# Optimization experiments

Measured on AMD Instinct MI355X. Metric: run time of the kernel, lower is better.

The kernel has to match this reference:

```python
import jax, jax.numpy as jnp
import numpy as np

N, E = 100000, 1600000          # nodes, edges
H, DH = 8, 256                  # heads, dim_hidden
D = DH // H                     # dim per head
NEG_SLOPE = 0.2                 # GAT leaky_relu slope
BETA = 0.5


def setup_inputs() -> dict:
    key = jax.random.key(0)
    ks = jax.random.split(key, 10)
    s = 1.0 / np.sqrt(DH)
    return {
        "x": jax.random.normal(ks[0], (N, DH), jnp.float32),
        "edge_index": jax.random.randint(ks[1], (2, E), 0, N, jnp.int32),
        "edge_attr": jax.random.uniform(ks[2], (E,), jnp.float32),
        # GAT params (no bias, add_self_loops=False)
        "Wg": jax.random.normal(ks[3], (DH, DH), jnp.float32) * s,
        "att_src": jax.random.normal(ks[4], (H, D), jnp.float32) * s,
        "att_dst": jax.random.normal(ks[5], (H, D), jnp.float32) * s,
        # h_lin
        "Wh": jax.random.normal(ks[6], (DH, DH), jnp.float32) * s,
        "bh": jnp.zeros((DH,), jnp.float32),
        # lin
        "Wl": jax.random.normal(ks[7], (DH, DH), jnp.float32) * s,
        "bl": jnp.zeros((DH,), jnp.float32),
        # LayerNorm
        "ln_g": jnp.ones((DH,), jnp.float32),
        "ln_b": jnp.zeros((DH,), jnp.float32),
        # beta gate (beta>=0 -> constant vector)
        "b_param": jnp.full((DH,), BETA, jnp.float32),
    }


def _layer_norm(v, g, b, eps=1e-5):
    mu = jnp.mean(v, axis=-1, keepdims=True)
    var = jnp.var(v, axis=-1, keepdims=True)
    return (v - mu) * jax.lax.rsqrt(var + eps) * g + b


def _weighted_gat(x, edge_index, edge_attr, Wg, att_src, att_dst):
    # GATConv with per-edge weights folded into the softmax numerator.
    xs = (x @ Wg).reshape(N, H, D)                       # [N,H,D]
    a_src = jnp.einsum("nhd,hd->nh", xs, att_src)        # [N,H]
    a_dst = jnp.einsum("nhd,hd->nh", xs, att_dst)
    src, dst = edge_index[0], edge_index[1]
    e = jax.nn.leaky_relu(a_src[src] + a_dst[dst], NEG_SLOPE)   # [E,H]
    m = jax.ops.segment_max(e, dst, num_segments=N)             # [N,H]
    m = jnp.where(jnp.isfinite(m), m, 0.0)                      # isolated nodes
    p = jnp.exp(e - m[dst]) * edge_attr[:, None]                # weighted exp
    denom = jax.ops.segment_sum(p, dst, num_segments=N)         # [N,H]
    alpha = p / (denom[dst] + 1e-16)                            # [E,H]
    msg = alpha[:, :, None] * xs[src]                           # [E,H,D]
    out = jax.ops.segment_sum(msg, dst, num_segments=N)         # [N,H,D]
    return out.reshape(N, DH)


def reference(x, edge_index, edge_attr, Wg, att_src, att_dst, Wh, bh, Wl, bl, ln_g, ln_b, b_param):
    x_in = x
    h = jax.nn.relu(x @ Wh + bh)
    xg = _weighted_gat(x, edge_index, edge_attr, Wg, att_src, att_dst) + (x @ Wl + bl)
    xg = jax.nn.relu(xg)                                  # dropout p=0 (eval)
    beta = b_param[None, :]
    out = (1.0 - beta) * _layer_norm(h * xg, ln_g, ln_b) + beta * xg
    return out + x_in                                     # residual=True
```

## Files before the change

### kernel.cpp

```cpp
#include <hip/hip_runtime.h>

typedef __attribute__((ext_vector_type(4))) float f32x4;
typedef __attribute__((ext_vector_type(8))) __bf16 bf16x8;

__device__ __forceinline__ unsigned short f2bf(float f) {
    return __builtin_bit_cast(unsigned short, (__bf16)f);
}
__device__ __forceinline__ float bf2f(unsigned short u) {
    return __builtin_bit_cast(float, (unsigned)u << 16);
}

__device__ __forceinline__ void gload16(const void* g, void* l) {
    __builtin_amdgcn_global_load_lds(
        (const __attribute__((address_space(1))) void*)g,
        (__attribute__((address_space(3))) void*)l, 16, 0, 0);
}

__global__ __launch_bounds__(256) void k_prep(
    const float* __restrict__ x, unsigned short* __restrict__ xb, long total, long totalPad,
    const float* __restrict__ Wg, const float* __restrict__ Wh, const float* __restrict__ Wl,
    unsigned short* __restrict__ wt,
    const int* __restrict__ dst, int E, int* __restrict__ deg,
    int nCvt, int nHist) {
    const int b = blockIdx.x;
    const int tid = threadIdx.x;
    if (b < nCvt) {
        long i = ((long)b * 256 + tid) * 4;
        if (i >= totalPad) return;
        if (i < total) {
            float4 v = *(const float4*)(x + i);
            ushort4 u;
            u.x = f2bf(v.x); u.y = f2bf(v.y); u.z = f2bf(v.z); u.w = f2bf(v.w);
            *(ushort4*)(xb + i) = u;
        } else {
            ushort4 u = {0, 0, 0, 0};
            *(ushort4*)(xb + i) = u;
        }
    } else if (b < nCvt + 768) {
        int t = (b - nCvt) * 256 + tid;
        int nn = t >> 8, k = t & 255;
        const float* W = (nn < 256) ? Wg : (nn < 512) ? Wh : Wl;
        wt[t] = f2bf(W[k * 256 + (nn & 255)]);
    } else {
        int bb = b - nCvt - 768;
        for (int e = bb * 256 + tid; e < E; e += nHist * 256)
            atomicAdd(&deg[dst[e]], 1);
    }
}

__global__ __launch_bounds__(256) void k_gemm(
    const unsigned short* __restrict__ A,
    const unsigned short* __restrict__ BT,
    unsigned short* __restrict__ xs, unsigned short* __restrict__ hb,
    unsigned short* __restrict__ xlb,
    const float* __restrict__ bh, const float* __restrict__ bl, int M, int nwg) {
    __shared__ unsigned short Al[128 * 32];
    __shared__ unsigned short Bl[128 * 32];
    const int bid = blockIdx.x;
    const int xcd = bid & 7, idx = bid >> 3;
    const int q = nwg >> 3, r = nwg & 7;
    const int wg = (xcd < r ? xcd * (q + 1) : r * (q + 1) + (xcd - r) * q) + idx;
    const int tm = wg / 6, tn = wg % 6;

    const int tid = threadIdx.x;
    const int lane = tid & 63;
    const int wave = tid >> 6;
    const int wm = (wave >> 1) * 64, wn = (wave & 1) * 64;

    f32x4 acc[4][4] = {};

    const int r0 = tid >> 2;
    const int ce = (tid & 3) * 8;
    const unsigned short* Ag = A + (size_t)tm * 128 * 256 + (size_t)r0 * 256 + ce;
    const unsigned short* Bg = BT + (size_t)tn * 128 * 256 + (size_t)r0 * 256 + ce;

    const int fr = lane & 15;
    const int ko = (lane >> 4) * 8;

    for (int ks = 0; ks < 8; ++ks) {
        const int k0 = ks * 32;
#pragma unroll
        for (int s = 0; s < 2; ++s) {
            gload16(Ag + (size_t)s * 64 * 256 + k0, (char*)Al + s * 4096 + wave * 1024);
            gload16(Bg + (size_t)s * 64 * 256 + k0, (char*)Bl + s * 4096 + wave * 1024);
        }
        __syncthreads();
        bf16x8 af[4], bfr[4];
#pragma unroll
        for (int i = 0; i < 4; ++i) {
            af[i]  = *(const bf16x8*)&Al[(wm + i * 16 + fr) * 32 + ko];
            bfr[i] = *(const bf16x8*)&Bl[(wn + i * 16 + fr) * 32 + ko];
        }
#pragma unroll
        for (int i = 0; i < 4; ++i)
#pragma unroll
            for (int j = 0; j < 4; ++j)
                acc[i][j] = __builtin_amdgcn_mfma_f32_16x16x32_bf16(af[i], bfr[j], acc[i][j], 0, 0, 0);
        __syncthreads();
    }

    const int colbase = tn * 128 + wn;
    const int rbase = tm * 128 + wm + (lane >> 4) * 4;
#pragma unroll
    for (int i = 0; i < 4; ++i) {
#pragma unroll
        for (int j = 0; j < 4; ++j) {
            const int cg = colbase + j * 16 + (lane & 15);
#pragma unroll
            for (int q2 = 0; q2 < 4; ++q2) {
                const int rg = rbase + i * 16 + q2;
                if (rg < M) {
                    float v = acc[i][j][q2];
                    if (cg < 256) {
                        xs[(size_t)rg * 256 + cg] = f2bf(v);
                    } else if (cg < 512) {
                        float t = v + bh[cg - 256];
                        hb[(size_t)rg * 256 + (cg - 256)] = f2bf(t > 0.f ? t : 0.f);
                    } else {
                        xlb[(size_t)rg * 256 + (cg - 512)] = f2bf(v + bl[cg - 512]);
                    }
                }
            }
        }
    }
}

__global__ __launch_bounds__(256) void k_attn(const unsigned short* __restrict__ xs,
                                              const float* __restrict__ att_src,
                                              const float* __restrict__ att_dst,
                                              float* __restrict__ a_src,
                                              float* __restrict__ a_dst, int N) {
    int t = blockIdx.x * 256 + threadIdx.x;
    int n = t >> 3, hh = t & 7;
    if (n >= N) return;
    const ushort4* xp = (const ushort4*)(xs + (size_t)n * 256 + hh * 32);
    const float4* sp = (const float4*)(att_src + hh * 32);
    const float4* dp = (const float4*)(att_dst + hh * 32);
    float sa = 0.f, sd = 0.f;
#pragma unroll
    for (int q = 0; q < 8; ++q) {
        ushort4 u = xp[q];
        float4 s = sp[q], d = dp[q];
        float v0 = bf2f(u.x), v1 = bf2f(u.y), v2 = bf2f(u.z), v3 = bf2f(u.w);
        sa += v0 * s.x + v1 * s.y + v2 * s.z + v3 * s.w;
        sd += v0 * d.x + v1 * d.y + v2 * d.z + v3 * d.w;
    }
    a_src[t] = sa;
    a_dst[t] = sd;
}

__global__ __launch_bounds__(256) void k_scan1(const int* __restrict__ deg, int* __restrict__ offs,
                                               int* __restrict__ bsum, int Npad) {
    __shared__ int s[256];
    int t = threadIdx.x;
    int i = blockIdx.x * 256 + t;
    int v = (i < Npad) ? deg[i] : 0;
    s[t] = v;
    __syncthreads();
#pragma unroll
    for (int off = 1; off < 256; off <<= 1) {
        int x = (t >= off) ? s[t - off] : 0;
        __syncthreads();
        s[t] += x;
        __syncthreads();
    }
    offs[i] = s[t] - v;
    if (t == 255) bsum[blockIdx.x] = s[255];
}

__global__ __launch_bounds__(512) void k_scan2(int* __restrict__ bsum, int nb) {
    __shared__ int s[512];
    int t = threadIdx.x;
    int v = (t < nb) ? bsum[t] : 0;
    s[t] = v;
    __syncthreads();
#pragma unroll
    for (int off = 1; off < 512; off <<= 1) {
        int x = (t >= off) ? s[t - off] : 0;
        __syncthreads();
        s[t] += x;
        __syncthreads();
    }
    if (t < nb) bsum[t] = s[t] - v;
}

__global__ __launch_bounds__(256) void k_scan3(int* __restrict__ offs, const int* __restrict__ bsum,
                                               int* __restrict__ cursor) {
    int i = blockIdx.x * 256 + threadIdx.x;
    int o = offs[i] + bsum[blockIdx.x];
    offs[i] = o;
    cursor[i] = o;
}

__global__ void k_edge(const int* __restrict__ ei, const float* __restrict__ ea, int E,
                       const float* __restrict__ a_src, const float* __restrict__ a_dst,
                       int* __restrict__ cursor, int* __restrict__ srcArr,
                       unsigned short* __restrict__ pvArr) {
    for (int e = blockIdx.x * blockDim.x + threadIdx.x; e < E; e += gridDim.x * blockDim.x) {
        const int s = ei[e];
        const int d = ei[(size_t)E + e];
        const float w = ea[e];
        const int pos = atomicAdd(&cursor[d], 1);
        const float4* As = (const float4*)(a_src + (size_t)s * 8);
        const float4* Ad = (const float4*)(a_dst + (size_t)d * 8);
        float4 s0 = As[0], s1 = As[1], d0 = Ad[0], d1 = Ad[1];
        float a[8] = {s0.x + d0.x, s0.y + d0.y, s0.z + d0.z, s0.w + d0.w,
                      s1.x + d1.x, s1.y + d1.y, s1.z + d1.z, s1.w + d1.w};
        unsigned pk[4];
#pragma unroll
        for (int h = 0; h < 4; ++h) {
            float lo = a[2 * h], hi = a[2 * h + 1];
            lo = (lo > 0.f) ? lo : 0.2f * lo;
            hi = (hi > 0.f) ? hi : 0.2f * hi;
            unsigned short plo = f2bf(__expf(lo) * w);
            unsigned short phi = f2bf(__expf(hi) * w);
            pk[h] = (unsigned)plo | ((unsigned)phi << 16);
        }
        srcArr[pos] = s;
        uint4 v = {pk[0], pk[1], pk[2], pk[3]};
        *(uint4*)(pvArr + (size_t)pos * 8) = v;
    }
}

__global__ __launch_bounds__(256) void k_agg(
    const int* __restrict__ offs, const int* __restrict__ deg,
    const int* __restrict__ srcArr, const unsigned short* __restrict__ pvArr,
    const unsigned short* __restrict__ xs, const unsigned short* __restrict__ hb,
    const unsigned short* __restrict__ xlb,
    const float* __restrict__ x, const float* __restrict__ ln_g, const float* __restrict__ ln_b,
    const float* __restrict__ beta, float* __restrict__ out, int N) {
    const int wave = threadIdx.x >> 6, lane = threadIdx.x & 63;
    const int n = blockIdx.x * 4 + wave;
    if (n >= N) return;
    const int start = __builtin_amdgcn_readfirstlane(offs[n]);
    const int dcount = __builtin_amdgcn_readfirstlane(deg[n]);
    const int head = lane >> 3;

    f32x4 acc = {0.f, 0.f, 0.f, 0.f};
    float dsum = 0.f;

    const int* sp = srcArr + start;
    const unsigned short* pp = pvArr + (size_t)start * 8 + head;
    const char* xsb = (const char*)xs;
    const unsigned rowoff = (unsigned)lane * 8;

    for (int e0 = 0; e0 < dcount; e0 += 8) {
        const int cnt = dcount - e0;
        int srcs[8];
        float pvv[8];
        ushort4 rows[8];
#pragma unroll
        for (int e = 0; e < 8; ++e)
            if (e < cnt) srcs[e] = sp[e0 + e];
#pragma unroll
        for (int e = 0; e < 8; ++e)
            if (e < cnt) {
                pvv[e] = bf2f(pp[(size_t)(e0 + e) * 8]);
                rows[e] = *(const ushort4*)(xsb + (size_t)(unsigned)srcs[e] * 512 + rowoff);
            }
#pragma unroll
        for (int e = 0; e < 8; ++e)
            if (e < cnt) {
                const float p = pvv[e];
                dsum += p;
                acc[0] += p * bf2f(rows[e].x);
                acc[1] += p * bf2f(rows[e].y);
                acc[2] += p * bf2f(rows[e].z);
                acc[3] += p * bf2f(rows[e].w);
            }
    }
    const float inv = 1.f / (dsum + 1e-16f);

    const size_t base = (size_t)n * 256 + lane * 4;
    ushort4 xlu = *(const ushort4*)(xlb + base);
    ushort4 hu = *(const ushort4*)(hb + base);
    f32x4 xg, t4;
    float s1 = 0.f, s2 = 0.f;
    const float xl0[4] = {bf2f(xlu.x), bf2f(xlu.y), bf2f(xlu.z), bf2f(xlu.w)};
    const float hv0[4] = {bf2f(hu.x), bf2f(hu.y), bf2f(hu.z), bf2f(hu.w)};
#pragma unroll
    for (int q = 0; q < 4; ++q) {
        float gg = acc[q] * inv + xl0[q];
        gg = gg > 0.f ? gg : 0.f;
        xg[q] = gg;
        float t = hv0[q] * gg;
        t4[q] = t;
        s1 += t;
        s2 += t * t;
    }
#pragma unroll
    for (int off = 32; off; off >>= 1) {
        s1 += __shfl_xor(s1, off);
        s2 += __shfl_xor(s2, off);
    }
    const float mu = s1 * (1.f / 256.f);
    const float var = s2 * (1.f / 256.f) - mu * mu;
    const float rs = rsqrtf(var + 1e-5f);

    f32x4 g4 = *(const f32x4*)(ln_g + lane * 4);
    f32x4 b4 = *(const f32x4*)(ln_b + lane * 4);
    f32x4 be = *(const f32x4*)(beta + lane * 4);
    f32x4 xin = *(const f32x4*)(x + base);
    f32x4 o;
#pragma unroll
    for (int q = 0; q < 4; ++q) {
        float ln = (t4[q] - mu) * rs * g4[q] + b4[q];
        o[q] = (1.f - be[q]) * ln + be[q] * xg[q] + xin[q];
    }
    *(f32x4*)(out + base) = o;
}

extern "C" void kernel_launch(void* const* d_in, const int* in_sizes, int n_in,
                              void* d_out, int out_size, void* d_ws, size_t ws_size,
                              hipStream_t stream) {
    const float* x = (const float*)d_in[0];
    const int* ei = (const int*)d_in[1];
    const float* ea = (const float*)d_in[2];
    const float* Wg = (const float*)d_in[3];
    const float* att_src = (const float*)d_in[4];
    const float* att_dst = (const float*)d_in[5];
    const float* Wh = (const float*)d_in[6];
    const float* bh = (const float*)d_in[7];
    const float* Wl = (const float*)d_in[8];
    const float* bl = (const float*)d_in[9];
    const float* ln_g = (const float*)d_in[10];
    const float* ln_b = (const float*)d_in[11];
    const float* beta = (const float*)d_in[12];
    float* out = (float*)d_out;

    const int DH = 256;
    const int N = in_sizes[0] / DH;
    const int E = in_sizes[2];
    const int Mpad = ((N + 127) / 128) * 128;
    const int Npad = ((N + 255) / 256) * 256;
    const int nscanb = Npad / 256;
    const int nwg = (Mpad / 128) * 6;
    const int nCvt = Mpad / 4;
    const int nHist = 2048;

    char* w = (char*)d_ws;
    auto take = [&](size_t bytes) -> char* {
        char* p = w;
        w += (bytes + 255) & ~(size_t)255;
        return p;
    };
    unsigned short* xs = (unsigned short*)take((size_t)N * DH * 2);
    unsigned short* hb = (unsigned short*)take((size_t)N * DH * 2);
    unsigned short* xlb = (unsigned short*)take((size_t)N * DH * 2);
    float* a_src = (float*)take((size_t)N * 8 * 4);
    float* a_dst = (float*)take((size_t)N * 8 * 4);
    unsigned short* xbf = (unsigned short*)take((size_t)Mpad * DH * 2);
    unsigned short* wt = (unsigned short*)take((size_t)768 * 256 * 2);
    int* deg = (int*)take((size_t)Npad * 4);
    int* offs = (int*)take((size_t)Npad * 4);
    int* cursor = (int*)take((size_t)Npad * 4);
    int* bsum = (int*)take(512 * 4);
    int* srcArr = (int*)take((size_t)E * 4 + 256);
    unsigned short* pvArr = (unsigned short*)take((size_t)E * 8 * 2 + 256);

    hipMemsetAsync(deg, 0, (size_t)Npad * 4, stream);

    k_prep<<<nCvt + 768 + nHist, 256, 0, stream>>>(x, xbf, (long)N * DH, (long)Mpad * DH,
                                                   Wg, Wh, Wl, wt, ei + E, E, deg, nCvt, nHist);

    k_scan1<<<nscanb, 256, 0, stream>>>(deg, offs, bsum, Npad);
    k_scan2<<<1, 512, 0, stream>>>(bsum, nscanb);
    k_scan3<<<nscanb, 256, 0, stream>>>(offs, bsum, cursor);

    k_gemm<<<nwg, 256, 0, stream>>>(xbf, wt, xs, hb, xlb, bh, bl, N, nwg);

    k_attn<<<(N * 8 + 255) / 256, 256, 0, stream>>>(xs, att_src, att_dst, a_src, a_dst, N);

    k_edge<<<2048, 256, 0, stream>>>(ei, ea, E, a_src, a_dst, cursor, srcArr, pvArr);

    k_agg<<<(N + 3) / 4, 256, 0, stream>>>(offs, deg, srcArr, pvArr,
                                           xs, hb, xlb, x, ln_g, ln_b, beta, out, N);
}
```

Measured before the change: 580.7 us.

## Pad CSR segments to 16 edges and load sources via wave shuffles

The scan now rounds each node's degree up to a multiple of 16. The padded edge arrays are zero-filled by memsets, so padding entries point at row 0 with zero weight. The aggregation loop can then process 16 edges per iteration with no bounds checks, loading source indices with one lane-parallel read and broadcasting them through __shfl. The residual now reads the bf16 copy of x instead of the fp32 input, which saves bandwidth but rounds the residual term to bf16. The cost is two extra large memsets, extra padded edge work (up to 15 dummy gathers per node against an average degree of about 16), and reduced precision in the residual.

Measured after the change: 593.7 us. 2.2% more time.

```diff
diff --git a/kernel.cpp b/kernel.cpp
--- a/kernel.cpp
+++ b/kernel.cpp
@@ -154,7 +154,7 @@
     __shared__ int s[256];
     int t = threadIdx.x;
     int i = blockIdx.x * 256 + t;
-    int v = (i < Npad) ? deg[i] : 0;
+    int v = (i < Npad) ? ((deg[i] + 15) & ~15) : 0;
     s[t] = v;
     __syncthreads();
 #pragma unroll
@@ -227,14 +227,16 @@
     const int* __restrict__ srcArr, const unsigned short* __restrict__ pvArr,
     const unsigned short* __restrict__ xs, const unsigned short* __restrict__ hb,
     const unsigned short* __restrict__ xlb,
-    const float* __restrict__ x, const float* __restrict__ ln_g, const float* __restrict__ ln_b,
+    const unsigned short* __restrict__ xbf, const float* __restrict__ ln_g,
+    const float* __restrict__ ln_b,
     const float* __restrict__ beta, float* __restrict__ out, int N) {
     const int wave = threadIdx.x >> 6, lane = threadIdx.x & 63;
     const int n = blockIdx.x * 4 + wave;
     if (n >= N) return;
-    const int start = __builtin_amdgcn_readfirstlane(offs[n]);
-    const int dcount = __builtin_amdgcn_readfirstlane(deg[n]);
+    const int start = offs[n];
+    const int dpad = (deg[n] + 15) & ~15;
     const int head = lane >> 3;
+    const int eSub = lane & 7;
 
     f32x4 acc = {0.f, 0.f, 0.f, 0.f};
     float dsum = 0.f;
@@ -244,40 +246,41 @@
     const char* xsb = (const char*)xs;
     const unsigned rowoff = (unsigned)lane * 8;
 
-    for (int e0 = 0; e0 < dcount; e0 += 8) {
-        const int cnt = dcount - e0;
-        int srcs[8];
-        float pvv[8];
-        ushort4 rows[8];
+    for (int g = 0; g < dpad; g += 16) {
+        const int sA = sp[g + eSub];
+        const int sB = sp[g + 8 + eSub];
+        ushort4 rows[16];
+        float pvv[16];
 #pragma unroll
         for (int e = 0; e < 8; ++e)
-            if (e < cnt) srcs[e] = sp[e0 + e];
+            rows[e] = *(const ushort4*)(xsb + (size_t)(unsigned)__shfl(sA, e) * 512 + rowoff);
 #pragma unroll
         for (int e = 0; e < 8; ++e)
-            if (e < cnt) {
-                pvv[e] = bf2f(pp[(size_t)(e0 + e) * 8]);
-                rows[e] = *(const ushort4*)(xsb + (size_t)(unsigned)srcs[e] * 512 + rowoff);
-            }
-#pragma unroll
-        for (int e = 0; e < 8; ++e)
-            if (e < cnt) {
-                const float p = pvv[e];
-                dsum += p;
-                acc[0] += p * bf2f(rows[e].x);
-                acc[1] += p * bf2f(rows[e].y);
-                acc[2] += p * bf2f(rows[e].z);
-                acc[3] += p * bf2f(rows[e].w);
-            }
+            rows[8 + e] = *(const ushort4*)(xsb + (size_t)(unsigned)__shfl(sB, e) * 512 + rowoff);
+#pragma unroll
+        for (int e = 0; e < 16; ++e)
+            pvv[e] = bf2f(pp[(size_t)(g + e) * 8]);
+#pragma unroll
+        for (int e = 0; e < 16; ++e) {
+            const float p = pvv[e];
+            dsum += p;
+            acc[0] += p * bf2f(rows[e].x);
+            acc[1] += p * bf2f(rows[e].y);
+            acc[2] += p * bf2f(rows[e].z);
+            acc[3] += p * bf2f(rows[e].w);
+        }
     }
     const float inv = 1.f / (dsum + 1e-16f);
 
     const size_t base = (size_t)n * 256 + lane * 4;
     ushort4 xlu = *(const ushort4*)(xlb + base);
     ushort4 hu = *(const ushort4*)(hb + base);
+    ushort4 xiu = *(const ushort4*)(xbf + base);
     f32x4 xg, t4;
     float s1 = 0.f, s2 = 0.f;
     const float xl0[4] = {bf2f(xlu.x), bf2f(xlu.y), bf2f(xlu.z), bf2f(xlu.w)};
     const float hv0[4] = {bf2f(hu.x), bf2f(hu.y), bf2f(hu.z), bf2f(hu.w)};
+    const float xi0[4] = {bf2f(xiu.x), bf2f(xiu.y), bf2f(xiu.z), bf2f(xiu.w)};
 #pragma unroll
     for (int q = 0; q < 4; ++q) {
         float gg = acc[q] * inv + xl0[q];
@@ -300,12 +303,11 @@
     f32x4 g4 = *(const f32x4*)(ln_g + lane * 4);
     f32x4 b4 = *(const f32x4*)(ln_b + lane * 4);
     f32x4 be = *(const f32x4*)(beta + lane * 4);
-    f32x4 xin = *(const f32x4*)(x + base);
     f32x4 o;
 #pragma unroll
     for (int q = 0; q < 4; ++q) {
         float ln = (t4[q] - mu) * rs * g4[q] + b4[q];
-        o[q] = (1.f - be[q]) * ln + be[q] * xg[q] + xin[q];
+        o[q] = (1.f - be[q]) * ln + be[q] * xg[q] + xi0[q];
     }
     *(f32x4*)(out + base) = o;
 }
@@ -337,6 +339,7 @@
     const int nwg = (Mpad / 128) * 6;
     const int nCvt = Mpad / 4;
     const int nHist = 2048;
+    const size_t Epad = (size_t)E + 16 * (size_t)N;
 
     char* w = (char*)d_ws;
     auto take = [&](size_t bytes) -> char* {
@@ -355,10 +358,12 @@
     int* offs = (int*)take((size_t)Npad * 4);
     int* cursor = (int*)take((size_t)Npad * 4);
     int* bsum = (int*)take(512 * 4);
-    int* srcArr = (int*)take((size_t)E * 4 + 256);
-    unsigned short* pvArr = (unsigned short*)take((size_t)E * 8 * 2 + 256);
+    int* srcArr = (int*)take(Epad * 4);
+    unsigned short* pvArr = (unsigned short*)take(Epad * 8 * 2);
 
     hipMemsetAsync(deg, 0, (size_t)Npad * 4, stream);
+    hipMemsetAsync(srcArr, 0, Epad * 4, stream);
+    hipMemsetAsync(pvArr, 0, Epad * 8 * 2, stream);
 
     k_prep<<<nCvt + 768 + nHist, 256, 0, stream>>>(x, xbf, (long)N * DH, (long)Mpad * DH,
                                                    Wg, Wh, Wl, wt, ei + E, E, deg, nCvt, nHist);
@@ -374,5 +379,5 @@
     k_edge<<<2048, 256, 0, stream>>>(ei, ea, E, a_src, a_dst, cursor, srcArr, pvArr);
 
     k_agg<<<(N + 3) / 4, 256, 0, stream>>>(offs, deg, srcArr, pvArr,
-                                           xs, hb, xlb, x, ln_g, ln_b, beta, out, N);
-}
+                                           xs, hb, xlb, xbf, ln_g, ln_b, beta, out, N);
+}
```
